# Kernel optimization log

Hardware: AMD Instinct MI355X
Metric: run time of the kernel (lower is better)

The kernel has to match this reference:

```python
import jax, jax.numpy as jnp
import numpy as np

LN2 = float(np.log(2.0))

def ssp(v):
    # PhysNet shifted softplus activation
    return jax.nn.softplus(v) - LN2

N, F, E, K, L = 50000, 128, 800000, 64, 3

def setup_inputs() -> dict:
    key = jax.random.key(0)
    ks = jax.random.split(key, 16)
    sc = 1.0 / np.sqrt(F)
    x = jax.random.normal(ks[0], (N, F), dtype=jnp.float32)
    rbf = jax.random.uniform(ks[1], (E, K), dtype=jnp.float32)
    idx_i = jnp.sort(jax.random.randint(ks[2], (E,), 0, N, dtype=jnp.int32))
    idx_j = jax.random.randint(ks[3], (E,), 0, N, dtype=jnp.int32)
    Wk2f = jax.random.normal(ks[4], (K, F), dtype=jnp.float32) / np.sqrt(K)
    Wi = jax.random.normal(ks[5], (F, F), dtype=jnp.float32) * sc
    bi = jnp.zeros((F,), jnp.float32)
    Wj = jax.random.normal(ks[6], (F, F), dtype=jnp.float32) * sc
    bj = jnp.zeros((F,), jnp.float32)
    Wr1 = jax.random.normal(ks[7], (L, F, F), dtype=jnp.float32) * sc
    br1 = jnp.zeros((L, F), jnp.float32)
    Wr2 = jax.random.normal(ks[8], (L, F, F), dtype=jnp.float32) * sc
    br2 = jnp.zeros((L, F), jnp.float32)
    Wf = jax.random.normal(ks[9], (F, F), dtype=jnp.float32) * sc
    bf = jnp.zeros((F,), jnp.float32)
    u = jnp.ones((F,), jnp.float32)
    return dict(x=x, rbf=rbf, Wk2f=Wk2f, Wi=Wi, bi=bi, Wj=Wj, bj=bj,
                Wr1=Wr1, br1=br1, Wr2=Wr2, br2=br2, Wf=Wf, bf=bf, u=u,
                idx_i=idx_i, idx_j=idx_j)

def reference(x, rbf, Wk2f, Wi, bi, Wj, bj, Wr1, br1, Wr2, br2, Wf, bf, u, idx_i, idx_j):
    xa = ssp(x)                                   # [N,F] (drop_rate=0 -> no dropout)
    g = rbf @ Wk2f                                # [E,F] rbf gate
    xi = ssp(xa @ Wi + bi)                        # [N,F]
    xj_all = ssp(xa @ Wj + bj)                    # [N,F]
    msgs = g * xj_all[idx_j]                      # [E,F] gather + gate
    xj = jax.ops.segment_sum(msgs, idx_i, num_segments=N)  # [N,F] scatter-reduce
    m = xi + xj
    for l in range(L):                            # PhysNet residual blocks
        y = ssp(m)
        m = m + ssp(y @ Wr1[l] + br1[l]) @ Wr2[l] + br2[l]
    m = ssp(m)
    return u * x + (m @ Wf + bf)
```

## Files before the change

### kernel.cpp

```cpp
#include <hip/hip_runtime.h>
#include <hip/hip_bf16.h>
#include <math.h>

typedef unsigned short u16;
typedef short bf16x8 __attribute__((ext_vector_type(8)));
typedef float f32x4 __attribute__((ext_vector_type(4)));

#define LN2F 0.693147180559945f

__device__ __forceinline__ float bf2f(u16 h) {
  union { unsigned int i; float f; } v; v.i = ((unsigned int)h) << 16; return v.f;
}
__device__ __forceinline__ u16 f2bf(float f) {
  union { float f; unsigned int i; } v; v.f = f;
  unsigned int x = v.i;
  return (u16)((x + 0x7fffu + ((x >> 16) & 1u)) >> 16);
}
__device__ __forceinline__ float sspf(float v) {
  return fmaxf(v, 0.0f) + __logf(1.0f + __expf(-fabsf(v))) - LN2F;
}

__global__ void probe_k(const u16* __restrict__ x, int* __restrict__ flag) {
  __shared__ int sf;
  if (threadIdx.x == 0) sf = 0;
  __syncthreads();
  int f = 0;
  for (int i = threadIdx.x; i < 4096; i += 256) {
    const unsigned e = (x[i] >> 7) & 0xFFu;
    if (e >= 0xC0u) f = 1;
  }
  if (f) atomicOr(&sf, 1);
  __syncthreads();
  if (threadIdx.x == 0) *flag = sf;
}

template<int NB>
__device__ __forceinline__ void copy_lin(const u16* __restrict__ g, u16* s, int tid) {
  constexpr int CH = NB / 16;
#pragma unroll
  for (int c = tid; c < CH; c += 256)
    *(bf16x8*)(s + (size_t)c * 8) = *(const bf16x8*)(g + (size_t)c * 8);
}

__device__ __forceinline__ void wload(const u16* __restrict__ g, bf16x8* w, int tid) {
#pragma unroll
  for (int p = 0; p < 8; ++p) w[p] = *(const bf16x8*)(g + (size_t)(tid + p * 256) * 8);
  if (tid < 128) w[8] = *(const bf16x8*)(g + (size_t)(2048 + tid) * 8);
}
__device__ __forceinline__ void wstore(u16* s, const bf16x8* w, int tid) {
#pragma unroll
  for (int p = 0; p < 8; ++p) *(bf16x8*)(s + (size_t)(tid + p * 256) * 8) = w[p];
  if (tid < 128) *(bf16x8*)(s + (size_t)(2048 + tid) * 8) = w[8];
}

template<int KSTEPS, int LDW>
__device__ __forceinline__ void mm_lds(const u16* sA, const u16* sW, f32x4* acc,
                                       int m16, int quad) {
#pragma unroll
  for (int s = 0; s < KSTEPS; ++s) {
    const int k0 = s * 32 + quad * 8;
    bf16x8 a = *(const bf16x8*)(sA + (size_t)m16 * LDW + k0);
#pragma unroll
    for (int t = 0; t < 8; ++t) {
      bf16x8 b = *(const bf16x8*)(sW + (size_t)(t * 16 + m16) * LDW + k0);
      acc[t] = __builtin_amdgcn_mfma_f32_16x16x32_bf16(a, b, acc[t], 0, 0, 0);
    }
  }
}

__global__ __launch_bounds__(256) void prep_k(
    const int* __restrict__ mode,
    const void* __restrict__ Wi, const void* __restrict__ Wj,
    const void* __restrict__ Wf, const void* __restrict__ Wk2f,
    const void* __restrict__ Wr1, const void* __restrict__ Wr2,
    u16* __restrict__ WT, int L)
{
  const int md = *mode;
  const int b = blockIdx.x, tid = threadIdx.x;
  const size_t esz = md ? 4 : 2;
  const void* src; u16* dst; int KD = 128, LDW = 136;
  if      (b == 0) { src = Wi;  dst = WT; }
  else if (b == 1) { src = Wj;  dst = WT + 17408; }
  else if (b == 2) { src = Wf;  dst = WT + 2 * 17408; }
  else if (b == 3) { src = Wk2f; dst = WT + (size_t)(3 + 2 * L) * 17408; KD = 64; LDW = 72; }
  else if (b < 4 + L) { int l = b - 4;     src = (const char*)Wr1 + (size_t)l * 16384 * esz; dst = WT + (size_t)(3 + l) * 17408; }
  else                { int l = b - 4 - L; src = (const char*)Wr2 + (size_t)l * 16384 * esz; dst = WT + (size_t)(3 + L + l) * 17408; }

  const int n  = tid & 127;
  const int kh = (tid >> 7) * (KD >> 1);
  if (md == 0) {
    for (int c = 0; c < (KD >> 4); ++c) {
      const int k0 = kh + c * 8;
      bf16x8 rv;
#pragma unroll
      for (int j = 0; j < 8; ++j)
        rv[j] = (short)((const u16*)src)[(size_t)(k0 + j) * 128 + n];
      *(bf16x8*)(dst + (size_t)n * LDW + k0) = rv;
    }
  } else {
    for (int c = 0; c < (KD >> 4); ++c) {
      const int k0 = kh + c * 8;
      bf16x8 rv;
#pragma unroll
      for (int j = 0; j < 8; ++j)
        rv[j] = (short)f2bf(((const float*)src)[(size_t)(k0 + j) * 128 + n]);
      *(bf16x8*)(dst + (size_t)n * LDW + k0) = rv;
    }
  }
}

__global__ __launch_bounds__(256) void in_k(
    const int* __restrict__ mode, const void* __restrict__ x,
    const u16* __restrict__ WiT, const u16* __restrict__ WjT,
    const void* __restrict__ bi, const void* __restrict__ bj,
    float* __restrict__ mb, u16* __restrict__ xjt, int N)
{
  const int md = *mode;
  __shared__ u16 sW[128 * 136];
  const int tid = threadIdx.x, lane = tid & 63, wave = tid >> 6;
  const int m16 = lane & 15, quad = lane >> 4;
  const int row_tile = blockIdx.x * 64 + wave * 16;
  int arow = row_tile + m16; if (arow >= N) arow = N - 1;

  bf16x8 af[4];
  if (md == 0) {
#pragma unroll
    for (int s = 0; s < 4; ++s) {
      const int k0 = s * 32 + quad * 8;
      bf16x8 raw = *(const bf16x8*)((const u16*)x + (size_t)arow * 128 + k0);
#pragma unroll
      for (int j = 0; j < 8; ++j) af[s][j] = (short)f2bf(sspf(bf2f((u16)raw[j])));
    }
  } else {
#pragma unroll
    for (int s = 0; s < 4; ++s) {
      const int k0 = s * 32 + quad * 8;
      const float* ap = (const float*)x + (size_t)arow * 128 + k0;
      float4 lo = *(const float4*)ap, hi = *(const float4*)(ap + 4);
      float v[8] = {lo.x, lo.y, lo.z, lo.w, hi.x, hi.y, hi.z, hi.w};
#pragma unroll
      for (int j = 0; j < 8; ++j) af[s][j] = (short)f2bf(sspf(v[j]));
    }
  }

  copy_lin<128 * 136 * 2>(WiT, sW, tid);
  __syncthreads();
  f32x4 aI[8], aJ[8];
#pragma unroll
  for (int t = 0; t < 8; ++t) aI[t] = (f32x4){0.f, 0.f, 0.f, 0.f};
  bf16x8 w[9];
  wload(WjT, w, tid);
#pragma unroll
  for (int s = 0; s < 4; ++s) {
    const int k0 = s * 32 + quad * 8;
#pragma unroll
    for (int t = 0; t < 8; ++t) {
      bf16x8 b = *(const bf16x8*)(sW + (size_t)(t * 16 + m16) * 136 + k0);
      aI[t] = __builtin_amdgcn_mfma_f32_16x16x32_bf16(af[s], b, aI[t], 0, 0, 0);
    }
  }
  __syncthreads();
  wstore(sW, w, tid);
  __syncthreads();
#pragma unroll
  for (int t = 0; t < 8; ++t) aJ[t] = (f32x4){0.f, 0.f, 0.f, 0.f};
#pragma unroll
  for (int s = 0; s < 4; ++s) {
    const int k0 = s * 32 + quad * 8;
#pragma unroll
    for (int t = 0; t < 8; ++t) {
      bf16x8 b = *(const bf16x8*)(sW + (size_t)(t * 16 + m16) * 136 + k0);
      aJ[t] = __builtin_amdgcn_mfma_f32_16x16x32_bf16(af[s], b, aJ[t], 0, 0, 0);
    }
  }

#pragma unroll
  for (int t = 0; t < 8; ++t) {
    const int col = t * 16 + m16;
    float biv, bjv;
    if (md == 0) { biv = bf2f(((const u16*)bi)[col]); bjv = bf2f(((const u16*)bj)[col]); }
    else         { biv = ((const float*)bi)[col];     bjv = ((const float*)bj)[col]; }
#pragma unroll
    for (int r = 0; r < 4; ++r) {
      const int ro = row_tile + quad * 4 + r;
      if (ro >= N) continue;
      const size_t off = (size_t)ro * 128 + col;
      mb[off]  = sspf(aI[t][r] + biv);
      xjt[off] = f2bf(sspf(aJ[t][r] + bjv));
    }
  }
}

__global__ __launch_bounds__(256) void edge_k(
    const int* __restrict__ mode,
    const void* __restrict__ rbf, const u16* __restrict__ WkT,
    const u16* __restrict__ xj_all, const int* __restrict__ idx_i,
    const int* __restrict__ idx_j, float* __restrict__ mb, int E)
{
  const int md = *mode;
  __shared__ u16 sW[128 * 72];
  __shared__ u16 sMsg[64][132];
  __shared__ int sIi[64];
  const int tid = threadIdx.x;
  const int e0 = blockIdx.x * 64;
  const int lane = tid & 63, wave = tid >> 6;
  const int m16 = lane & 15, quad = lane >> 4;
  const int lebase = wave * 16 + quad * 4;

  if (tid < 64) sIi[tid] = (e0 + tid < E) ? idx_i[e0 + tid] : -1;
  int jrow[4];
#pragma unroll
  for (int r = 0; r < 4; ++r) {
    const int e = e0 + lebase + r;
    jrow[r] = (e < E) ? idx_j[e] : 0;
  }

  bf16x8 w[5];
#pragma unroll
  for (int p = 0; p < 4; ++p) w[p] = *(const bf16x8*)(WkT + (size_t)(tid + p * 256) * 8);
  if (tid < 128) w[4] = *(const bf16x8*)(WkT + (size_t)(1024 + tid) * 8);

  int er = e0 + wave * 16 + m16; if (er >= E) er = E - 1;
  bf16x8 rb[2];
  if (md == 0) {
    const u16* p = (const u16*)rbf + (size_t)er * 64 + quad * 8;
    rb[0] = *(const bf16x8*)p;
    rb[1] = *(const bf16x8*)(p + 32);
  } else {
    const float* p = (const float*)rbf + (size_t)er * 64 + quad * 8;
    float4 a0 = *(const float4*)p,        a1 = *(const float4*)(p + 4);
    float4 a2 = *(const float4*)(p + 32), a3 = *(const float4*)(p + 36);
    rb[0][0] = f2bf(a0.x); rb[0][1] = f2bf(a0.y); rb[0][2] = f2bf(a0.z); rb[0][3] = f2bf(a0.w);
    rb[0][4] = f2bf(a1.x); rb[0][5] = f2bf(a1.y); rb[0][6] = f2bf(a1.z); rb[0][7] = f2bf(a1.w);
    rb[1][0] = f2bf(a2.x); rb[1][1] = f2bf(a2.y); rb[1][2] = f2bf(a2.z); rb[1][3] = f2bf(a2.w);
    rb[1][4] = f2bf(a3.x); rb[1][5] = f2bf(a3.y); rb[1][6] = f2bf(a3.z); rb[1][7] = f2bf(a3.w);
  }

  u16 xg[8][4];
#pragma unroll
  for (int r = 0; r < 4; ++r) {
    const u16* xr = xj_all + (size_t)jrow[r] * 128 + m16;
#pragma unroll
    for (int t = 0; t < 8; ++t) xg[t][r] = xr[t * 16];
  }

#pragma unroll
  for (int p = 0; p < 4; ++p) *(bf16x8*)(sW + (size_t)(tid + p * 256) * 8) = w[p];
  if (tid < 128) *(bf16x8*)(sW + (size_t)(1024 + tid) * 8) = w[4];
  __syncthreads();

  f32x4 acc[8];
#pragma unroll
  for (int t = 0; t < 8; ++t) acc[t] = (f32x4){0.f, 0.f, 0.f, 0.f};
#pragma unroll
  for (int s = 0; s < 2; ++s) {
    const int k0 = s * 32 + quad * 8;
#pragma unroll
    for (int t = 0; t < 8; ++t) {
      bf16x8 b = *(const bf16x8*)(sW + (size_t)(t * 16 + m16) * 72 + k0);
      acc[t] = __builtin_amdgcn_mfma_f32_16x16x32_bf16(rb[s], b, acc[t], 0, 0, 0);
    }
  }

#pragma unroll
  for (int t = 0; t < 8; ++t) {
    const int col = t * 16 + m16;
#pragma unroll
    for (int r = 0; r < 4; ++r) {
      const float xvf = (e0 + lebase + r < E) ? bf2f(xg[t][r]) : 0.f;
      sMsg[lebase + r][col] = f2bf(acc[t][r] * xvf);
    }
  }
  __syncthreads();

  const int scol = tid & 127;
  const int sbeg = (tid >> 7) * 32;
  float sum = 0.f;
  int cur = sIi[sbeg];
#pragma unroll 4
  for (int r = 0; r < 32; ++r) {
    const int node = sIi[sbeg + r];
    if (node != cur) {
      if (cur >= 0) atomicAdd(&mb[(size_t)cur * 128 + scol], sum);
      sum = 0.f; cur = node;
    }
    sum += bf2f(sMsg[sbeg + r][scol]);
  }
  if (cur >= 0) atomicAdd(&mb[(size_t)cur * 128 + scol], sum);
}

__global__ __launch_bounds__(256) void resid_k(
    const int* __restrict__ mode, const float* __restrict__ mb,
    const u16* __restrict__ WT,
    const void* __restrict__ br1, const void* __restrict__ br2,
    const void* __restrict__ bfv, const void* __restrict__ x,
    const void* __restrict__ u, void* __restrict__ out, int N, int L)
{
  const int md = *mode;
  __shared__ u16 sW[128 * 136];
  __shared__ u16 sM[128 * 136];
  const int tid = threadIdx.x, lane = tid & 63, wave = tid >> 6;
  const int m16 = lane & 15, quad = lane >> 4;
  const int rb0 = blockIdx.x * 128;

  f32x4 m[2][8];
#pragma unroll
  for (int s = 0; s < 2; ++s) {
#pragma unroll
    for (int t = 0; t < 8; ++t) {
      const int col = t * 16 + m16;
#pragma unroll
      for (int r = 0; r < 4; ++r) {
        int ro = rb0 + s * 64 + wave * 16 + quad * 4 + r;
        if (ro >= N) ro = N - 1;
        m[s][t][r] = mb[(size_t)ro * 128 + col];
      }
    }
  }

  const u16* W1T = WT + (size_t)3 * 17408;
  const u16* W2T = WT + (size_t)(3 + L) * 17408;
  bf16x8 w[9];

  for (int l = 0; l < L; ++l) {
    wload(W1T + (size_t)l * 17408, w, tid);
#pragma unroll
    for (int s = 0; s < 2; ++s)
#pragma unroll
      for (int t = 0; t < 8; ++t) {
        const int col = t * 16 + m16;
#pragma unroll
        for (int r = 0; r < 4; ++r)
          sM[(size_t)(s * 64 + wave * 16 + quad * 4 + r) * 136 + col] = f2bf(sspf(m[s][t][r]));
      }
    wstore(sW, w, tid);
    __syncthreads();

    f32x4 a1[2][8];
#pragma unroll
    for (int s = 0; s < 2; ++s) {
#pragma unroll
      for (int t = 0; t < 8; ++t) a1[s][t] = (f32x4){0.f, 0.f, 0.f, 0.f};
      mm_lds<4, 136>(sM + (size_t)(s * 64 + wave * 16) * 136, sW, a1[s], m16, quad);
    }
    __syncthreads();

    wload(W2T + (size_t)l * 17408, w, tid);
#pragma unroll
    for (int s = 0; s < 2; ++s)
#pragma unroll
      for (int t = 0; t < 8; ++t) {
        const int col = t * 16 + m16;
        float b1v;
        if (md == 0) b1v = bf2f(((const u16*)br1)[(size_t)l * 128 + col]);
        else         b1v = ((const float*)br1)[(size_t)l * 128 + col];
#pragma unroll
        for (int r = 0; r < 4; ++r)
          sM[(size_t)(s * 64 + wave * 16 + quad * 4 + r) * 136 + col] = f2bf(sspf(a1[s][t][r] + b1v));
      }
    wstore(sW, w, tid);
    __syncthreads();

#pragma unroll
    for (int s = 0; s < 2; ++s)
      mm_lds<4, 136>(sM + (size_t)(s * 64 + wave * 16) * 136, sW, m[s], m16, quad);
#pragma unroll
    for (int t = 0; t < 8; ++t) {
      float b2v;
      if (md == 0) b2v = bf2f(((const u16*)br2)[(size_t)l * 128 + t * 16 + m16]);
      else         b2v = ((const float*)br2)[(size_t)l * 128 + t * 16 + m16];
#pragma unroll
      for (int s = 0; s < 2; ++s)
#pragma unroll
        for (int r = 0; r < 4; ++r) m[s][t][r] += b2v;
    }
    __syncthreads();
  }

  wload(WT + (size_t)2 * 17408, w, tid);
#pragma unroll
  for (int s = 0; s < 2; ++s)
#pragma unroll
    for (int t = 0; t < 8; ++t) {
      const int col = t * 16 + m16;
#pragma unroll
      for (int r = 0; r < 4; ++r)
        sM[(size_t)(s * 64 + wave * 16 + quad * 4 + r) * 136 + col] = f2bf(sspf(m[s][t][r]));
    }
  wstore(sW, w, tid);
  __syncthreads();

  f32x4 o[2][8];
#pragma unroll
  for (int s = 0; s < 2; ++s) {
#pragma unroll
    for (int t = 0; t < 8; ++t) o[s][t] = (f32x4){0.f, 0.f, 0.f, 0.f};
    mm_lds<4, 136>(sM + (size_t)(s * 64 + wave * 16) * 136, sW, o[s], m16, quad);
  }

#pragma unroll
  for (int t = 0; t < 8; ++t) {
    const int col = t * 16 + m16;
    float bv, uvv;
    if (md == 0) { bv = bf2f(((const u16*)bfv)[col]); uvv = bf2f(((const u16*)u)[col]); }
    else         { bv = ((const float*)bfv)[col];     uvv = ((const float*)u)[col]; }
#pragma unroll
    for (int s = 0; s < 2; ++s)
#pragma unroll
      for (int r = 0; r < 4; ++r) {
        const int ro = rb0 + s * 64 + wave * 16 + quad * 4 + r;
        if (ro >= N) continue;
        const size_t off = (size_t)ro * 128 + col;
        if (md == 0) ((u16*)out)[off]  = f2bf(uvv * bf2f(((const u16*)x)[off]) + o[s][t][r] + bv);
        else         ((float*)out)[off] = uvv * ((const float*)x)[off] + o[s][t][r] + bv;
      }
  }
}

extern "C" void kernel_launch(void* const* d_in, const int* in_sizes, int n_in,
                              void* d_out, int out_size, void* d_ws, size_t ws_size,
                              hipStream_t stream)
{
  const void* x    = d_in[0];
  const void* rbf  = d_in[1];
  const void* Wk2f = d_in[2];
  const void* Wi   = d_in[3];
  const void* bi   = d_in[4];
  const void* Wj   = d_in[5];
  const void* bj   = d_in[6];
  const void* Wr1  = d_in[7];
  const void* br1  = d_in[8];
  const void* Wr2  = d_in[9];
  const void* br2  = d_in[10];
  const void* Wf   = d_in[11];
  const void* bfv  = d_in[12];
  const void* uv   = d_in[13];
  const int* idx_i = (const int*)d_in[14];
  const int* idx_j = (const int*)d_in[15];

  const int N = in_sizes[0] / 128;
  const int E = in_sizes[14];
  const int L = in_sizes[7] / (128 * 128);

  int* flag = (int*)d_ws;
  char* wsb = (char*)d_ws + 16;
  const size_t avail = ws_size > 16 ? ws_size - 16 : 0;

  const size_t needW  = ((size_t)(3 + 2 * L) * 17408 + 9216) * 2;
  const size_t needWA = (needW + 255) & ~(size_t)255;
  u16* WT = (u16*)wsb;
  char* wsb2 = wsb + needWA;
  const size_t avail2 = (avail > needWA) ? avail - needWA : 0;

  const size_t needF = (size_t)N * 512;
  const size_t needH = (size_t)N * 256;

  float* mb; u16* xjt;
  if (avail2 >= needF + needH) { mb = (float*)wsb2; xjt = (u16*)(wsb2 + needF); }
  else if (avail2 >= needF)    { mb = (float*)wsb2; xjt = (u16*)d_out; }
  else                         { mb = (float*)d_out; xjt = (u16*)wsb2; }

  const dim3 blk(256);
  const int gridN = (N + 63) / 64;
  const int gridR = (N + 127) / 128;
  const int gridE = (E + 63) / 64;

  probe_k<<<1, 256, 0, stream>>>((const u16*)x, flag);
  prep_k<<<4 + 2 * L, blk, 0, stream>>>(flag, Wi, Wj, Wf, Wk2f, Wr1, Wr2, WT, L);
  in_k<<<gridN, blk, 0, stream>>>(flag, x, WT, WT + 17408, bi, bj, mb, xjt, N);
  edge_k<<<gridE, blk, 0, stream>>>(flag, rbf, WT + (size_t)(3 + 2 * L) * 17408,
                                    xjt, idx_i, idx_j, mb, E);
  resid_k<<<gridR, blk, 0, stream>>>(flag, mb, WT, br1, br2, bfv, x, uv, d_out, N, L);
}
```

Before: 549.7 us.

## Drop LDS weight staging in edge kernel and halve residual block rows

```diff
diff --git a/kernel.cpp b/kernel.cpp
--- a/kernel.cpp
+++ b/kernel.cpp
@@ -191,14 +191,13 @@
   }
 }
 
-__global__ __launch_bounds__(256) void edge_k(
+__global__ __launch_bounds__(256, 6) void edge_k(
     const int* __restrict__ mode,
     const void* __restrict__ rbf, const u16* __restrict__ WkT,
     const u16* __restrict__ xj_all, const int* __restrict__ idx_i,
     const int* __restrict__ idx_j, float* __restrict__ mb, int E)
 {
   const int md = *mode;
-  __shared__ u16 sW[128 * 72];
   __shared__ u16 sMsg[64][132];
   __shared__ int sIi[64];
   const int tid = threadIdx.x;
@@ -214,11 +213,6 @@
     const int e = e0 + lebase + r;
     jrow[r] = (e < E) ? idx_j[e] : 0;
   }
-
-  bf16x8 w[5];
-#pragma unroll
-  for (int p = 0; p < 4; ++p) w[p] = *(const bf16x8*)(WkT + (size_t)(tid + p * 256) * 8);
-  if (tid < 128) w[4] = *(const bf16x8*)(WkT + (size_t)(1024 + tid) * 8);
 
   int er = e0 + wave * 16 + m16; if (er >= E) er = E - 1;
   bf16x8 rb[2];
@@ -244,20 +238,15 @@
     for (int t = 0; t < 8; ++t) xg[t][r] = xr[t * 16];
   }
 
-#pragma unroll
-  for (int p = 0; p < 4; ++p) *(bf16x8*)(sW + (size_t)(tid + p * 256) * 8) = w[p];
-  if (tid < 128) *(bf16x8*)(sW + (size_t)(1024 + tid) * 8) = w[4];
-  __syncthreads();
-
   f32x4 acc[8];
 #pragma unroll
   for (int t = 0; t < 8; ++t) acc[t] = (f32x4){0.f, 0.f, 0.f, 0.f};
+  const u16* wp = WkT + (size_t)m16 * 72 + quad * 8;
 #pragma unroll
   for (int s = 0; s < 2; ++s) {
-    const int k0 = s * 32 + quad * 8;
-#pragma unroll
-    for (int t = 0; t < 8; ++t) {
-      bf16x8 b = *(const bf16x8*)(sW + (size_t)(t * 16 + m16) * 72 + k0);
+#pragma unroll
+    for (int t = 0; t < 8; ++t) {
+      bf16x8 b = *(const bf16x8*)(wp + (size_t)(t * 16) * 72 + s * 32);
       acc[t] = __builtin_amdgcn_mfma_f32_16x16x32_bf16(rb[s], b, acc[t], 0, 0, 0);
     }
   }
@@ -298,23 +287,20 @@
 {
   const int md = *mode;
   __shared__ u16 sW[128 * 136];
-  __shared__ u16 sM[128 * 136];
+  __shared__ u16 sM[64 * 136];
   const int tid = threadIdx.x, lane = tid & 63, wave = tid >> 6;
   const int m16 = lane & 15, quad = lane >> 4;
-  const int rb0 = blockIdx.x * 128;
-
-  f32x4 m[2][8];
-#pragma unroll
-  for (int s = 0; s < 2; ++s) {
-#pragma unroll
-    for (int t = 0; t < 8; ++t) {
-      const int col = t * 16 + m16;
-#pragma unroll
-      for (int r = 0; r < 4; ++r) {
-        int ro = rb0 + s * 64 + wave * 16 + quad * 4 + r;
-        if (ro >= N) ro = N - 1;
-        m[s][t][r] = mb[(size_t)ro * 128 + col];
-      }
+  const int rbase = blockIdx.x * 64 + wave * 16 + quad * 4;
+  u16* sMw = sM + (size_t)(wave * 16) * 136;
+
+  f32x4 m[8];
+#pragma unroll
+  for (int t = 0; t < 8; ++t) {
+    const int col = t * 16 + m16;
+#pragma unroll
+    for (int r = 0; r < 4; ++r) {
+      int ro = rbase + r; if (ro >= N) ro = N - 1;
+      m[t][r] = mb[(size_t)ro * 128 + col];
     }
   }
 
@@ -325,78 +311,62 @@
   for (int l = 0; l < L; ++l) {
     wload(W1T + (size_t)l * 17408, w, tid);
 #pragma unroll
-    for (int s = 0; s < 2; ++s)
-#pragma unroll
-      for (int t = 0; t < 8; ++t) {
-        const int col = t * 16 + m16;
-#pragma unroll
-        for (int r = 0; r < 4; ++r)
-          sM[(size_t)(s * 64 + wave * 16 + quad * 4 + r) * 136 + col] = f2bf(sspf(m[s][t][r]));
-      }
+    for (int t = 0; t < 8; ++t) {
+      const int col = t * 16 + m16;
+#pragma unroll
+      for (int r = 0; r < 4; ++r)
+        sM[(size_t)(wave * 16 + quad * 4 + r) * 136 + col] = f2bf(sspf(m[t][r]));
+    }
     wstore(sW, w, tid);
     __syncthreads();
 
-    f32x4 a1[2][8];
-#pragma unroll
-    for (int s = 0; s < 2; ++s) {
-#pragma unroll
-      for (int t = 0; t < 8; ++t) a1[s][t] = (f32x4){0.f, 0.f, 0.f, 0.f};
-      mm_lds<4, 136>(sM + (size_t)(s * 64 + wave * 16) * 136, sW, a1[s], m16, quad);
-    }
+    f32x4 a1[8];
+#pragma unroll
+    for (int t = 0; t < 8; ++t) a1[t] = (f32x4){0.f, 0.f, 0.f, 0.f};
+    mm_lds<4, 136>(sMw, sW, a1, m16, quad);
     __syncthreads();
 
     wload(W2T + (size_t)l * 17408, w, tid);
 #pragma unroll
-    for (int s = 0; s < 2; ++s)
-#pragma unroll
-      for (int t = 0; t < 8; ++t) {
-        const int col = t * 16 + m16;
-        float b1v;
-        if (md == 0) b1v = bf2f(((const u16*)br1)[(size_t)l * 128 + col]);
-        else         b1v = ((const float*)br1)[(size_t)l * 128 + col];
-#pragma unroll
-        for (int r = 0; r < 4; ++r)
-          sM[(size_t)(s * 64 + wave * 16 + quad * 4 + r) * 136 + col] = f2bf(sspf(a1[s][t][r] + b1v));
-      }
+    for (int t = 0; t < 8; ++t) {
+      const int col = t * 16 + m16;
+      float b1v;
+      if (md == 0) b1v = bf2f(((const u16*)br1)[(size_t)l * 128 + col]);
+      else         b1v = ((const float*)br1)[(size_t)l * 128 + col];
+#pragma unroll
+      for (int r = 0; r < 4; ++r)
+        sM[(size_t)(wave * 16 + quad * 4 + r) * 136 + col] = f2bf(sspf(a1[t][r] + b1v));
+    }
     wstore(sW, w, tid);
     __syncthreads();
 
-#pragma unroll
-    for (int s = 0; s < 2; ++s)
-      mm_lds<4, 136>(sM + (size_t)(s * 64 + wave * 16) * 136, sW, m[s], m16, quad);
+    mm_lds<4, 136>(sMw, sW, m, m16, quad);
 #pragma unroll
     for (int t = 0; t < 8; ++t) {
       float b2v;
       if (md == 0) b2v = bf2f(((const u16*)br2)[(size_t)l * 128 + t * 16 + m16]);
       else         b2v = ((const float*)br2)[(size_t)l * 128 + t * 16 + m16];
 #pragma unroll
-      for (int s = 0; s < 2; ++s)
-#pragma unroll
-        for (int r = 0; r < 4; ++r) m[s][t][r] += b2v;
+      for (int r = 0; r < 4; ++r) m[t][r] += b2v;
     }
     __syncthreads();
   }
 
   wload(WT + (size_t)2 * 17408, w, tid);
 #pragma unroll
-  for (int s = 0; s < 2; ++s)
-#pragma unroll
-    for (int t = 0; t < 8; ++t) {
-      const int col = t * 16 + m16;
-#pragma unroll
-      for (int r = 0; r < 4; ++r)
-        sM[(size_t)(s * 64 + wave * 16 + quad * 4 + r) * 136 + col] = f2bf(sspf(m[s][t][r]));
-    }
+  for (int t = 0; t < 8; ++t) {
+    const int col = t * 16 + m16;
+#pragma unroll
+    for (int r = 0; r < 4; ++r)
+      sM[(size_t)(wave * 16 + quad * 4 + r) * 136 + col] = f2bf(sspf(m[t][r]));
+  }
   wstore(sW, w, tid);
   __syncthreads();
 
-  f32x4 o[2][8];
-#pragma unroll
-  for (int s = 0; s < 2; ++s) {
-#pragma unroll
-    for (int t = 0; t < 8; ++t) o[s][t] = (f32x4){0.f, 0.f, 0.f, 0.f};
-    mm_lds<4, 136>(sM + (size_t)(s * 64 + wave * 16) * 136, sW, o[s], m16, quad);
-  }
+  f32x4 o[8];
+#pragma unroll
+  for (int t = 0; t < 8; ++t) o[t] = (f32x4){0.f, 0.f, 0.f, 0.f};
+  mm_lds<4, 136>(sMw, sW, o, m16, quad);
 
 #pragma unroll
   for (int t = 0; t < 8; ++t) {
@@ -405,15 +375,13 @@
     if (md == 0) { bv = bf2f(((const u16*)bfv)[col]); uvv = bf2f(((const u16*)u)[col]); }
     else         { bv = ((const float*)bfv)[col];     uvv = ((const float*)u)[col]; }
 #pragma unroll
-    for (int s = 0; s < 2; ++s)
-#pragma unroll
-      for (int r = 0; r < 4; ++r) {
-        const int ro = rb0 + s * 64 + wave * 16 + quad * 4 + r;
-        if (ro >= N) continue;
-        const size_t off = (size_t)ro * 128 + col;
-        if (md == 0) ((u16*)out)[off]  = f2bf(uvv * bf2f(((const u16*)x)[off]) + o[s][t][r] + bv);
-        else         ((float*)out)[off] = uvv * ((const float*)x)[off] + o[s][t][r] + bv;
-      }
+    for (int r = 0; r < 4; ++r) {
+      const int ro = rbase + r;
+      if (ro >= N) continue;
+      const size_t off = (size_t)ro * 128 + col;
+      if (md == 0) ((u16*)out)[off]  = f2bf(uvv * bf2f(((const u16*)x)[off]) + o[t][r] + bv);
+      else         ((float*)out)[off] = uvv * ((const float*)x)[off] + o[t][r] + bv;
+    }
   }
 }
 
@@ -462,7 +430,6 @@
 
   const dim3 blk(256);
   const int gridN = (N + 63) / 64;
-  const int gridR = (N + 127) / 128;
   const int gridE = (E + 63) / 64;
 
   probe_k<<<1, 256, 0, stream>>>((const u16*)x, flag);
@@ -470,5 +437,5 @@
   in_k<<<gridN, blk, 0, stream>>>(flag, x, WT, WT + 17408, bi, bj, mb, xjt, N);
   edge_k<<<gridE, blk, 0, stream>>>(flag, rbf, WT + (size_t)(3 + 2 * L) * 17408,
                                     xjt, idx_i, idx_j, mb, E);
-  resid_k<<<gridR, blk, 0, stream>>>(flag, mb, WT, br1, br2, bfv, x, uv, d_out, N, L);
-}
+  resid_k<<<gridN, blk, 0, stream>>>(flag, mb, WT, br1, br2, bfv, x, uv, d_out, N, L);
+}
```

New measurement: 550.6 us. No clear change (+0.2%).
